# Performance work log

Hardware: AMD Instinct MI355X
Metric: run time of the kernel (lower is better)

## Reference

```python
import jax, jax.numpy as jnp
import numpy as np

D_MODEL = 1024
NUM_HEADS = 16
HEAD_DIM = D_MODEL // NUM_HEADS
BATCH = 2
SEQ = 2048


def setup_inputs() -> dict:
    key = jax.random.key(0)
    ks = jax.random.split(key, 9)
    s = 1.0 / np.sqrt(D_MODEL)
    inp = {
        "x": jax.random.normal(ks[0], (BATCH, SEQ, D_MODEL), dtype=jnp.float32),
        "mask": jnp.ones((BATCH, SEQ), dtype=jnp.int32),
        "Wq": jax.random.uniform(ks[1], (D_MODEL, D_MODEL), jnp.float32, -s, s),
        "bq": jax.random.uniform(ks[2], (D_MODEL,), jnp.float32, -s, s),
        "Wk": jax.random.uniform(ks[3], (D_MODEL, D_MODEL), jnp.float32, -s, s),
        "bk": jax.random.uniform(ks[4], (D_MODEL,), jnp.float32, -s, s),
        "Wv": jax.random.uniform(ks[5], (D_MODEL, D_MODEL), jnp.float32, -s, s),
        "bv": jax.random.uniform(ks[6], (D_MODEL,), jnp.float32, -s, s),
        "Wo": jax.random.uniform(ks[7], (D_MODEL, D_MODEL), jnp.float32, -s, s),
        "bo": jax.random.uniform(ks[8], (D_MODEL,), jnp.float32, -s, s),
    }
    return inp


def reference(x, mask, Wq, bq, Wk, bk, Wv, bv, Wo, bo):
    B, S, D = x.shape
    H, Hd = NUM_HEADS, HEAD_DIM
    # torch Linear: y = x @ W.T + b ; then reshape to [B, H, S, Hd]
    def proj(W, b):
        return (x @ W.T + b).reshape(B, S, H, Hd).transpose(0, 2, 1, 3)
    Q = proj(Wq, bq)
    K = proj(Wk, bk)
    V = proj(Wv, bv)
    scale = 1.0 / jnp.sqrt(jnp.asarray(Hd, dtype=x.dtype))
    scores = jnp.einsum("bhqd,bhkd->bhqk", Q, K) * scale  # [B,H,S,S]
    # mask [B,S] -> broadcast over query positions; masked_fill(mask==0, -1e9)
    scores = jnp.where(mask[:, None, None, :] == 0, jnp.asarray(-1e9, x.dtype), scores)
    attn = jax.nn.softmax(scores, axis=-1)
    context = jnp.einsum("bhqk,bhkd->bhqd", attn, V)
    context = context.transpose(0, 2, 1, 3).reshape(B, S, D)
    return context @ Wo.T + bo
```

## Files before the change

kernel.cpp:

```cpp
#include <hip/hip_runtime.h>
#include <hip/hip_bf16.h>
#include <cstdint>

#define D_MODEL 1024
#define NUM_HEADS 16
#define HEAD_DIM 64
#define BATCH 2
#define SEQ 2048
#define MROWS (BATCH * SEQ)

typedef __attribute__((ext_vector_type(8))) short bf16x8;
typedef __attribute__((ext_vector_type(4))) float f32x4;
typedef unsigned short u16;

#define QSCALE (0.125f * 1.44269504f)

#if __has_builtin(__builtin_amdgcn_exp2f)
#define EXP2F(x) __builtin_amdgcn_exp2f(x)
#else
#define EXP2F(x) exp2f(x)
#endif

static __device__ __forceinline__ u16 f2bf(float f) {
    unsigned int u = __float_as_uint(f);
    unsigned int lsb = (u >> 16) & 1u;
    u += 0x7fffu + lsb;
    return (u16)(u >> 16);
}

#if __has_builtin(__builtin_amdgcn_cvt_pk_bf16_f32)
static __device__ __forceinline__ unsigned pkbf(float a, float b) {
    typedef __attribute__((ext_vector_type(2))) __bf16 bf2;
    union { bf2 v; unsigned u; } cv;
    cv.v = __builtin_amdgcn_cvt_pk_bf16_f32(a, b);
    return cv.u;
}
#else
static __device__ __forceinline__ unsigned pkbf(float a, float b) {
    unsigned ua = (__float_as_uint(a) + 0x8000u) >> 16;
    unsigned ub = (__float_as_uint(b) + 0x8000u) & 0xffff0000u;
    return ua | ub;
}
#endif

static __device__ __forceinline__ void gload_lds16(const void* g, void* l) {
    __builtin_amdgcn_global_load_lds((const __attribute__((address_space(1))) unsigned int*)g,
                                     (__attribute__((address_space(3))) unsigned int*)l,
                                     16, 0, 0);
}

__global__ void cvt_all(const float* __restrict__ x,
                        const float* __restrict__ w0, const float* __restrict__ w1,
                        const float* __restrict__ w2, const float* __restrict__ w3,
                        u16* __restrict__ base) {
    const int which = blockIdx.y;
    const int NE = D_MODEL * D_MODEL;
    const float* s;
    if (which < 4)      s = x + (size_t)which * NE;
    else if (which == 4) s = w0;
    else if (which == 5) s = w1;
    else if (which == 6) s = w2;
    else                 s = w3;
    u16* dst = base + (size_t)which * NE;
    const int i = (blockIdx.x * blockDim.x + threadIdx.x) * 4;
    float4 v = *(const float4*)(s + i);
    ushort4 o;
    o.x = f2bf(v.x); o.y = f2bf(v.y); o.z = f2bf(v.z); o.w = f2bf(v.w);
    *(ushort4*)(dst + i) = o;
}

template<int BN, int MODE>
__global__ __launch_bounds__(256, 3)
void gemm_staged(const u16* __restrict__ A, const u16* __restrict__ W,
                 const float* __restrict__ b0, const float* __restrict__ b1,
                 const float* __restrict__ b2,
                 u16* __restrict__ o0, u16* __restrict__ o1, u16* __restrict__ o2,
                 float* __restrict__ of, int K, int N) {
    constexpr int WN = BN / 2;
    constexpr int NJ = WN / 16;
    __shared__ __align__(16) u16 As[128 * 64];
    __shared__ __align__(16) u16 Bs[BN * 64];

    const int lane = threadIdx.x & 63;
    const int w    = threadIdx.x >> 6;
    const int quad = lane >> 4;
    const int l16  = lane & 15;
    const int wm = w >> 1, wn = w & 1;

    const u16* Ablk = A + (size_t)(blockIdx.y * 128) * K;
    const u16* Wblk = W + (size_t)(blockIdx.x * BN) * K;

    const int srow = lane >> 3;
    const int scol = lane & 7;

    f32x4 acc[4][NJ];
#pragma unroll
    for (int i = 0; i < 4; ++i)
#pragma unroll
        for (int j = 0; j < NJ; ++j) acc[i][j] = (f32x4){0.f, 0.f, 0.f, 0.f};

    for (int kb0 = 0; kb0 < K; kb0 += 64) {
        __syncthreads();
#pragma unroll
        for (int t = 0; t < 4; ++t) {
            const int r  = w * 32 + t * 8 + srow;
            const int cg = scol ^ (r & 7);
            gload_lds16(Ablk + (size_t)r * K + kb0 + cg * 8, &As[(w * 32 + t * 8) * 64]);
        }
#pragma unroll
        for (int t = 0; t < BN / 32; ++t) {
            const int r  = w * (BN / 4) + t * 8 + srow;
            const int cg = scol ^ (r & 7);
            gload_lds16(Wblk + (size_t)r * K + kb0 + cg * 8, &Bs[(w * (BN / 4) + t * 8) * 64]);
        }
        __syncthreads();
#pragma unroll
        for (int ks = 0; ks < 2; ++ks) {
            bf16x8 a[4], b[NJ];
#pragma unroll
            for (int i = 0; i < 4; ++i) {
                const int ra = wm * 64 + 16 * i + l16;
                a[i] = *(const bf16x8*)&As[ra * 64 + ((ks * 4 + quad) ^ (ra & 7)) * 8];
            }
#pragma unroll
            for (int j = 0; j < NJ; ++j) {
                const int rb = wn * WN + 16 * j + l16;
                b[j] = *(const bf16x8*)&Bs[rb * 64 + ((ks * 4 + quad) ^ (rb & 7)) * 8];
            }
#pragma unroll
            for (int i = 0; i < 4; ++i)
#pragma unroll
                for (int j = 0; j < NJ; ++j)
                    acc[i][j] = __builtin_amdgcn_mfma_f32_16x16x32_bf16(a[i], b[j], acc[i][j], 0, 0, 0);
        }
    }

    const int mbase = blockIdx.y * 128 + wm * 64;
    const int nbase = blockIdx.x * BN + wn * WN;

    if (MODE == 0) {
#pragma unroll
        for (int j = 0; j < NJ; ++j) {
            const int gn = nbase + 16 * j + l16;
            const int which = gn >> 10, rem = gn & 1023;
            const float bv = (which == 0 ? b0 : which == 1 ? b1 : b2)[rem];
            u16* dst = (which == 0) ? o0 : (which == 1) ? o1 : o2;
            const float scl = (which == 0) ? QSCALE : 1.0f;
            const int h = rem >> 6, d = rem & 63;
#pragma unroll
            for (int i = 0; i < 4; ++i)
#pragma unroll
                for (int r = 0; r < 4; ++r) {
                    const int gm = mbase + 16 * i + quad * 4 + r;
                    const int bb = gm >> 11, s = gm & 2047;
                    dst[(((size_t)(bb * NUM_HEADS + h) * SEQ) + s) * 64 + d] =
                        f2bf((acc[i][j][r] + bv) * scl);
                }
        }
    } else {
#pragma unroll
        for (int j = 0; j < NJ; ++j) {
            const int gn = nbase + 16 * j + l16;
            const float bv = b0[gn];
#pragma unroll
            for (int i = 0; i < 4; ++i)
#pragma unroll
                for (int r = 0; r < 4; ++r) {
                    const int gm = mbase + 16 * i + quad * 4 + r;
                    of[(size_t)gm * N + gn] = acc[i][j][r] + bv;
                }
        }
    }
}

__global__ void transpose_v(const u16* __restrict__ V, u16* __restrict__ VT) {
    __shared__ __align__(16) u16 T[64 * 64];
    const int t    = threadIdx.x;
    const int lane = t & 63, w = t >> 6;
    const int bh   = blockIdx.x & 31, sblk = blockIdx.x >> 5;
    const u16* src = V + ((size_t)bh * SEQ + sblk * 64) * 64;

#pragma unroll
    for (int p = 0; p < 2; ++p) {
        const int r = p * 32 + w * 8 + (lane >> 3);
        const int c = lane & 7;
        bf16x8 v = *(const bf16x8*)(src + r * 64 + c * 8);
        *(bf16x8*)&T[r * 64 + ((c ^ (r & 7)) * 8)] = v;
    }
    __syncthreads();
    u16* dst = VT + ((size_t)bh * 64) * SEQ + sblk * 64;
#pragma unroll
    for (int p = 0; p < 2; ++p) {
        const int r  = p * 32 + w * 8 + (lane >> 3);
        const int sc = lane & 7;
        union { u16 u[8]; bf16x8 v; } pk;
#pragma unroll
        for (int j = 0; j < 8; ++j)
            pk.u[j] = T[(sc * 8 + j) * 64 + (((r >> 3) ^ j) * 8) + (r & 7)];
        *(bf16x8*)(dst + (size_t)r * SEQ + sc * 8) = pk.v;
    }
}

__global__ __launch_bounds__(512, 2)
void attn_kernel(const u16* __restrict__ Q, const u16* __restrict__ K,
                 const u16* __restrict__ VT, const int* __restrict__ mask,
                 u16* __restrict__ ctx) {
    __shared__ __align__(16) u16 Ks[2][64 * 64];
    __shared__ __align__(16) u16 Vs[2][64 * 64];
    __shared__ __align__(16) u16 Ps[8][32 * 72];

    const int lane = threadIdx.x & 63;
    const int w    = threadIdx.x >> 6;
    const int quad = lane >> 4;
    const int l16  = lane & 15;

    const int bh = blockIdx.x & 31;
    const int qb = blockIdx.x >> 5;
    const int b  = bh >> 4;
    const int h  = bh & 15;
    const int qbase = qb * 256 + w * 32;

    const u16* Qh = Q + (size_t)bh * SEQ * 64;
    const u16* Kh = K + (size_t)bh * SEQ * 64;
    const u16* Vh = VT + (size_t)bh * 64 * SEQ;
    const int* mrow = mask + b * SEQ;

    const int srow = lane >> 3;
    const int scol = lane & 7;
    const int cg   = scol ^ srow;

    gload_lds16(Kh + (size_t)(8 * w + srow) * 64 + cg * 8, &Ks[0][(8 * w) * 64]);
    gload_lds16(Vh + (size_t)(8 * w + srow) * SEQ + cg * 8, &Vs[0][(8 * w) * 64]);

    bf16x8 qf[2][2];
#pragma unroll
    for (int iq = 0; iq < 2; ++iq)
#pragma unroll
        for (int ks = 0; ks < 2; ++ks)
            qf[iq][ks] = *(const bf16x8*)(Qh + (size_t)(qbase + 16 * iq + l16) * 64 + 32 * ks + quad * 8);

    f32x4 o[2][4];
#pragma unroll
    for (int iq = 0; iq < 2; ++iq)
#pragma unroll
        for (int id = 0; id < 4; ++id) o[iq][id] = (f32x4){0.f, 0.f, 0.f, 0.f};
    float lst[2] = {0.f, 0.f};

    unsigned short* myp = &Ps[w][0];
    const int rowsel = (lane & 48) | (quad * 4);

#pragma unroll 2
    for (int kb = 0; kb < 32; ++kb) {
        const int cur = kb & 1;
        __syncthreads();

        if (kb != 31) {
            const int kn = (kb + 1) * 64;
            gload_lds16(Kh + (size_t)(kn + 8 * w + srow) * 64 + cg * 8,
                        &Ks[cur ^ 1][(8 * w) * 64]);
            gload_lds16(Vh + (size_t)(8 * w + srow) * SEQ + kn + cg * 8,
                        &Vs[cur ^ 1][(8 * w) * 64]);
        }

        const int kstart = kb * 64;
        const int mv = mrow[kstart + lane];
        const bool clean = (__ballot(mv != 0) == ~0ull);

        bf16x8 kf[4][2];
#pragma unroll
        for (int ik = 0; ik < 4; ++ik) {
            const int row = 16 * ik + l16;
#pragma unroll
            for (int ks = 0; ks < 2; ++ks)
                kf[ik][ks] = *(const bf16x8*)&Ks[cur][row * 64 + ((4 * ks + quad) ^ (row & 7)) * 8];
        }

        f32x4 s[4][2];
#pragma unroll
        for (int ik = 0; ik < 4; ++ik)
#pragma unroll
            for (int iq = 0; iq < 2; ++iq) {
                f32x4 t = (f32x4){0.f, 0.f, 0.f, 0.f};
                t = __builtin_amdgcn_mfma_f32_16x16x32_bf16(kf[ik][0], qf[iq][0], t, 0, 0, 0);
                t = __builtin_amdgcn_mfma_f32_16x16x32_bf16(kf[ik][1], qf[iq][1], t, 0, 0, 0);
                s[ik][iq] = t;
            }

        bf16x8 vf[4][2];
#pragma unroll
        for (int id = 0; id < 4; ++id) {
            const int row = 16 * id + l16;
#pragma unroll
            for (int ks = 0; ks < 2; ++ks)
                vf[id][ks] = *(const bf16x8*)&Vs[cur][row * 64 + ((4 * ks + quad) ^ (row & 7)) * 8];
        }

        if (!clean) {
#pragma unroll
            for (int ik = 0; ik < 4; ++ik) {
                int4 mk = *(const int4*)(mrow + kstart + 16 * ik + quad * 4);
                const int* mp = (const int*)&mk;
#pragma unroll
                for (int r = 0; r < 4; ++r) {
                    const bool keep = (mp[r] != 0);
#pragma unroll
                    for (int iq = 0; iq < 2; ++iq)
                        s[ik][iq][r] = keep ? s[ik][iq][r] : -1e9f;
                }
            }
        }

#pragma unroll
        for (int iq = 0; iq < 2; ++iq) {
            float rs = 0.f;
#pragma unroll
            for (int ik = 0; ik < 4; ++ik) {
                const float p0 = EXP2F(fminf(s[ik][iq][0], 80.f));
                const float p1 = EXP2F(fminf(s[ik][iq][1], 80.f));
                const float p2 = EXP2F(fminf(s[ik][iq][2], 80.f));
                const float p3 = EXP2F(fminf(s[ik][iq][3], 80.f));
                rs += (p0 + p1) + (p2 + p3);
                uint2 pk;
                pk.x = pkbf(p0, p1);
                pk.y = pkbf(p2, p3);
                *(uint2*)(myp + (16 * iq + l16) * 72 + 16 * ik + quad * 4) = pk;
            }
            rs += __shfl_xor(rs, 16, 64);
            rs += __shfl_xor(rs, 32, 64);
            lst[iq] += rs;
        }

#pragma unroll
        for (int ks = 0; ks < 2; ++ks) {
            bf16x8 pf[2];
#pragma unroll
            for (int iq = 0; iq < 2; ++iq)
                pf[iq] = *(const bf16x8*)(myp + (16 * iq + l16) * 72 + 32 * ks + quad * 8);
#pragma unroll
            for (int iq = 0; iq < 2; ++iq)
#pragma unroll
                for (int id = 0; id < 4; ++id)
                    o[iq][id] = __builtin_amdgcn_mfma_f32_16x16x32_bf16(pf[iq], vf[id][ks], o[iq][id], 0, 0, 0);
        }
    }

#pragma unroll
    for (int iq = 0; iq < 2; ++iq) {
        float linv[4];
#pragma unroll
        for (int r = 0; r < 4; ++r) linv[r] = 1.f / __shfl(lst[iq], rowsel + r, 64);
#pragma unroll
        for (int id = 0; id < 4; ++id)
#pragma unroll
            for (int r = 0; r < 4; ++r) {
                const int q = qbase + 16 * iq + quad * 4 + r;
                const int d = 16 * id + l16;
                ctx[((size_t)(b * SEQ + q)) * D_MODEL + h * 64 + d] = f2bf(o[iq][id][r] * linv[r]);
            }
    }
}

extern "C" void kernel_launch(void* const* d_in, const int* in_sizes, int n_in,
                              void* d_out, int out_size, void* d_ws, size_t ws_size,
                              hipStream_t stream) {
    const float* x    = (const float*)d_in[0];
    const int*   mask = (const int*)d_in[1];
    const float* Wq   = (const float*)d_in[2];
    const float* bq   = (const float*)d_in[3];
    const float* Wk   = (const float*)d_in[4];
    const float* bk   = (const float*)d_in[5];
    const float* Wv   = (const float*)d_in[6];
    const float* bv   = (const float*)d_in[7];
    const float* Wo   = (const float*)d_in[8];
    const float* bo   = (const float*)d_in[9];

    u16* xb  = (u16*)d_ws;
    u16* wqb = xb  + (size_t)MROWS * D_MODEL;
    u16* wob = wqb + (size_t)3 * D_MODEL * D_MODEL;
    u16* Qb  = wob + (size_t)D_MODEL * D_MODEL;
    u16* Kb  = Qb  + (size_t)MROWS * D_MODEL;
    u16* VTb = Kb  + (size_t)MROWS * D_MODEL;
    u16* ctx = VTb + (size_t)MROWS * D_MODEL;

    cvt_all<<<dim3(D_MODEL * D_MODEL / 1024, 8), 256, 0, stream>>>(
        x, Wq, Wk, Wv, Wo, xb);

    gemm_staged<128, 0><<<dim3(3 * D_MODEL / 128, MROWS / 128), 256, 0, stream>>>(
        xb, wqb, bq, bk, bv, Qb, Kb, ctx, nullptr, D_MODEL, 3 * D_MODEL);

    transpose_v<<<BATCH * NUM_HEADS * (SEQ / 64), 256, 0, stream>>>(ctx, VTb);

    attn_kernel<<<BATCH * NUM_HEADS * (SEQ / 256), 512, 0, stream>>>(Qb, Kb, VTb, mask, ctx);

    gemm_staged<64, 1><<<dim3(D_MODEL / 64, MROWS / 128), 256, 0, stream>>>(
        ctx, wob, bo, nullptr, nullptr, nullptr, nullptr, nullptr,
        (float*)d_out, D_MODEL, D_MODEL);
}
```

Baseline: 203.7 us.

## Split attention key range across two wave groups per block and merge partial outputs

Each 512-thread block now covers 128 queries instead of 256. Its two groups of four waves each process half of the key sequence, and the groups merge their unnormalized outputs and row sums through shared memory at the end. This doubles the attention grid to give more blocks per CU and better latency hiding. K/V tiles are now prefetched through registers instead of direct global-to-LDS loads, each group has a single shared buffer, and each iteration has two barriers. The occupancy hint is raised to 4, which may force register pressure or spills.

```diff
diff --git a/kernel.cpp b/kernel.cpp
--- a/kernel.cpp
+++ b/kernel.cpp
@@ -201,7 +201,7 @@
     }
 }
 
-__global__ __launch_bounds__(512, 2)
+__global__ __launch_bounds__(512, 4)
 void attn_kernel(const u16* __restrict__ Q, const u16* __restrict__ K,
                  const u16* __restrict__ VT, const int* __restrict__ mask,
                  u16* __restrict__ ctx) {
@@ -211,6 +211,8 @@
 
     const int lane = threadIdx.x & 63;
     const int w    = threadIdx.x >> 6;
+    const int g    = w >> 2;
+    const int ws4  = w & 3;
     const int quad = lane >> 4;
     const int l16  = lane & 15;
 
@@ -218,19 +220,25 @@
     const int qb = blockIdx.x >> 5;
     const int b  = bh >> 4;
     const int h  = bh & 15;
-    const int qbase = qb * 256 + w * 32;
+    const int qbase = qb * 128 + ws4 * 32;
 
     const u16* Qh = Q + (size_t)bh * SEQ * 64;
     const u16* Kh = K + (size_t)bh * SEQ * 64;
     const u16* Vh = VT + (size_t)bh * 64 * SEQ;
     const int* mrow = mask + b * SEQ;
+    const int kofs = g * 1024;
 
     const int srow = lane >> 3;
     const int scol = lane & 7;
     const int cg   = scol ^ srow;
 
-    gload_lds16(Kh + (size_t)(8 * w + srow) * 64 + cg * 8, &Ks[0][(8 * w) * 64]);
-    gload_lds16(Vh + (size_t)(8 * w + srow) * SEQ + cg * 8, &Vs[0][(8 * w) * 64]);
+    uint4 kreg[2], vreg[2];
+#pragma unroll
+    for (int t2 = 0; t2 < 2; ++t2) {
+        const int rl = 16 * ws4 + 8 * t2 + srow;
+        kreg[t2] = *(const uint4*)(Kh + (size_t)(kofs + rl) * 64 + cg * 8);
+        vreg[t2] = *(const uint4*)(Vh + (size_t)rl * SEQ + kofs + cg * 8);
+    }
 
     bf16x8 qf[2][2];
 #pragma unroll
@@ -249,20 +257,27 @@
     unsigned short* myp = &Ps[w][0];
     const int rowsel = (lane & 48) | (quad * 4);
 
-#pragma unroll 2
-    for (int kb = 0; kb < 32; ++kb) {
-        const int cur = kb & 1;
+    for (int t = 0; t < 16; ++t) {
         __syncthreads();
 
-        if (kb != 31) {
-            const int kn = (kb + 1) * 64;
-            gload_lds16(Kh + (size_t)(kn + 8 * w + srow) * 64 + cg * 8,
-                        &Ks[cur ^ 1][(8 * w) * 64]);
-            gload_lds16(Vh + (size_t)(8 * w + srow) * SEQ + kn + cg * 8,
-                        &Vs[cur ^ 1][(8 * w) * 64]);
-        }
-
-        const int kstart = kb * 64;
+#pragma unroll
+        for (int t2 = 0; t2 < 2; ++t2) {
+            const int rl = 16 * ws4 + 8 * t2 + srow;
+            *(uint4*)&Ks[g][rl * 64 + scol * 8] = kreg[t2];
+            *(uint4*)&Vs[g][rl * 64 + scol * 8] = vreg[t2];
+        }
+        if (t != 15) {
+            const int kn = kofs + (t + 1) * 64;
+#pragma unroll
+            for (int t2 = 0; t2 < 2; ++t2) {
+                const int rl = 16 * ws4 + 8 * t2 + srow;
+                kreg[t2] = *(const uint4*)(Kh + (size_t)(kn + rl) * 64 + cg * 8);
+                vreg[t2] = *(const uint4*)(Vh + (size_t)rl * SEQ + kn + cg * 8);
+            }
+        }
+        __syncthreads();
+
+        const int kstart = kofs + t * 64;
         const int mv = mrow[kstart + lane];
         const bool clean = (__ballot(mv != 0) == ~0ull);
 
@@ -272,7 +287,7 @@
             const int row = 16 * ik + l16;
 #pragma unroll
             for (int ks = 0; ks < 2; ++ks)
-                kf[ik][ks] = *(const bf16x8*)&Ks[cur][row * 64 + ((4 * ks + quad) ^ (row & 7)) * 8];
+                kf[ik][ks] = *(const bf16x8*)&Ks[g][row * 64 + ((4 * ks + quad) ^ (row & 7)) * 8];
         }
 
         f32x4 s[4][2];
@@ -280,10 +295,10 @@
         for (int ik = 0; ik < 4; ++ik)
 #pragma unroll
             for (int iq = 0; iq < 2; ++iq) {
-                f32x4 t = (f32x4){0.f, 0.f, 0.f, 0.f};
-                t = __builtin_amdgcn_mfma_f32_16x16x32_bf16(kf[ik][0], qf[iq][0], t, 0, 0, 0);
-                t = __builtin_amdgcn_mfma_f32_16x16x32_bf16(kf[ik][1], qf[iq][1], t, 0, 0, 0);
-                s[ik][iq] = t;
+                f32x4 t0 = (f32x4){0.f, 0.f, 0.f, 0.f};
+                t0 = __builtin_amdgcn_mfma_f32_16x16x32_bf16(kf[ik][0], qf[iq][0], t0, 0, 0, 0);
+                t0 = __builtin_amdgcn_mfma_f32_16x16x32_bf16(kf[ik][1], qf[iq][1], t0, 0, 0, 0);
+                s[ik][iq] = t0;
             }
 
         bf16x8 vf[4][2];
@@ -292,7 +307,7 @@
             const int row = 16 * id + l16;
 #pragma unroll
             for (int ks = 0; ks < 2; ++ks)
-                vf[id][ks] = *(const bf16x8*)&Vs[cur][row * 64 + ((4 * ks + quad) ^ (row & 7)) * 8];
+                vf[id][ks] = *(const bf16x8*)&Vs[g][row * 64 + ((4 * ks + quad) ^ (row & 7)) * 8];
         }
 
         if (!clean) {
@@ -344,19 +359,38 @@
         }
     }
 
-#pragma unroll
-    for (int iq = 0; iq < 2; ++iq) {
-        float linv[4];
-#pragma unroll
-        for (int r = 0; r < 4; ++r) linv[r] = 1.f / __shfl(lst[iq], rowsel + r, 64);
-#pragma unroll
-        for (int id = 0; id < 4; ++id)
-#pragma unroll
-            for (int r = 0; r < 4; ++r) {
-                const int q = qbase + 16 * iq + quad * 4 + r;
-                const int d = 16 * id + l16;
-                ctx[((size_t)(b * SEQ + q)) * D_MODEL + h * 64 + d] = f2bf(o[iq][id][r] * linv[r]);
-            }
+    __syncthreads();
+    float* Ot = (float*)&Ps[0][0];
+    float* lt = (float*)&Ks[0][0];
+    if (g == 1) {
+#pragma unroll
+        for (int iq = 0; iq < 2; ++iq) {
+#pragma unroll
+            for (int id = 0; id < 4; ++id)
+                *(f32x4*)&Ot[ws4 * 2048 + (iq * 4 + id) * 256 + lane * 4] = o[iq][id];
+            if (quad == 0) lt[ws4 * 32 + iq * 16 + l16] = lst[iq];
+        }
+    }
+    __syncthreads();
+    if (g == 0) {
+#pragma unroll
+        for (int iq = 0; iq < 2; ++iq) {
+            const float ltot = lst[iq] + lt[ws4 * 32 + iq * 16 + l16];
+            float linv[4];
+#pragma unroll
+            for (int r = 0; r < 4; ++r) linv[r] = 1.f / __shfl(ltot, rowsel + r, 64);
+#pragma unroll
+            for (int id = 0; id < 4; ++id) {
+                const f32x4 o2 = *(const f32x4*)&Ot[ws4 * 2048 + (iq * 4 + id) * 256 + lane * 4];
+#pragma unroll
+                for (int r = 0; r < 4; ++r) {
+                    const int q = qbase + 16 * iq + quad * 4 + r;
+                    const int d = 16 * id + l16;
+                    ctx[((size_t)(b * SEQ + q)) * D_MODEL + h * 64 + d] =
+                        f2bf((o[iq][id][r] + o2[r]) * linv[r]);
+                }
+            }
+        }
     }
 }
 
@@ -390,7 +424,7 @@
 
     transpose_v<<<BATCH * NUM_HEADS * (SEQ / 64), 256, 0, stream>>>(ctx, VTb);
 
-    attn_kernel<<<BATCH * NUM_HEADS * (SEQ / 256), 512, 0, stream>>>(Qb, Kb, VTb, mask, ctx);
+    attn_kernel<<<BATCH * NUM_HEADS * (SEQ / 128), 512, 0, stream>>>(Qb, Kb, VTb, mask, ctx);
 
     gemm_staged<64, 1><<<dim3(D_MODEL / 64, MROWS / 128), 256, 0, stream>>>(
         ctx, wob, bo, nullptr, nullptr, nullptr, nullptr, nullptr,
```

New measurement: 353.9 us. 1.74x slower.
